# Kernel tuning notes

Measured on AMD Instinct MI355X. Metric: run time of the kernel, lower is better.

## Reference

```python
import jax, jax.numpy as jnp
import numpy as np

LN_EPS = 1e-5  # torch.nn.LayerNorm default


def setup_inputs() -> dict:
    key = jax.random.key(0)
    k1, k2 = jax.random.split(key)
    N, D_IN, D_OUT, G = 4096, 512, 512, 32
    x = jax.random.normal(k1, (N, D_IN), dtype=jnp.float32)
    ln_w = jnp.ones((D_IN,), dtype=jnp.float32)
    ln_b = jnp.zeros((D_IN,), dtype=jnp.float32)
    scale = 1.0 / (np.sqrt(D_IN) * np.sqrt(G))
    fouriercoeffs = jax.random.normal(k2, (2, D_OUT, D_IN, G), dtype=jnp.float32) * scale
    bias = jnp.zeros((1, D_OUT), dtype=jnp.float32)
    return {"x": x, "ln_w": ln_w, "ln_b": ln_b, "fouriercoeffs": fouriercoeffs, "bias": bias}


def reference(x, ln_w, ln_b, fouriercoeffs, bias):
    # LayerNorm over last dim
    mu = jnp.mean(x, axis=-1, keepdims=True)
    var = jnp.mean((x - mu) ** 2, axis=-1, keepdims=True)
    xn = (x - mu) * jax.lax.rsqrt(var + LN_EPS) * ln_w + ln_b
    G = fouriercoeffs.shape[-1]
    k = jnp.arange(1, G + 1, dtype=xn.dtype)           # [G]
    arg = xn[:, :, None] * k                            # [N, D_in, G]
    c = jnp.cos(arg)
    s = jnp.sin(arg)
    # contraction over (inputdim, gridsize) -> GEMM-shaped einsum
    y = jnp.einsum('big,oig->bo', c, fouriercoeffs[0])
    y = y + jnp.einsum('big,oig->bo', s, fouriercoeffs[1])
    y = y + bias
    return y
```

## Files before the change

### kernel.cpp

```cpp
#include <hip/hip_runtime.h>
#include <hip/hip_bf16.h>


#define N_ROWS 4096
#define D_IN   512
#define D_OUT  512
#define KT     16384
#define BM 128
#define BN 128
#define SPLITK 4

typedef short short8 __attribute__((ext_vector_type(8)));
typedef float float4v __attribute__((ext_vector_type(4)));

__device__ inline unsigned int pack2bf(float a, float b) {
    __hip_bfloat162 h = __float22bfloat162_rn(make_float2(a, b));
    union { __hip_bfloat162 h; unsigned int u; } cv;
    cv.h = h;
    return cv.u;
}

__device__ inline unsigned short bf16_1(float a) {
    union { float f; unsigned int u; } cv;
    cv.f = a;
    unsigned int r = (cv.u + 0x7fff + ((cv.u >> 16) & 1)) >> 16;
    return (unsigned short)r;
}

__global__ __launch_bounds__(256) void ln_stats(const float* __restrict__ x,
        float2* __restrict__ mu_rs) {
    const int t = threadIdx.x;
    const int row = blockIdx.x * 4 + (t >> 6);
    const int lane = t & 63;
    const float4* xr = (const float4*)(x + (size_t)row * D_IN);
    float4 a = xr[lane];
    float4 c = xr[lane + 64];
    float s = a.x + a.y + a.z + a.w + c.x + c.y + c.z + c.w;
    float q = a.x * a.x + a.y * a.y + a.z * a.z + a.w * a.w
            + c.x * c.x + c.y * c.y + c.z * c.z + c.w * c.w;
    #pragma unroll
    for (int off = 32; off > 0; off >>= 1) {
        s += __shfl_down(s, off, 64);
        q += __shfl_down(q, off, 64);
    }
    if (lane == 0) {
        float mu = s * (1.f / D_IN);
        float var = q * (1.f / D_IN) - mu * mu;
        mu_rs[row] = make_float2(mu, rsqrtf(var + 1e-5f));
    }
}

__global__ __launch_bounds__(256) void feat_seed(const float* __restrict__ x,
        const float* __restrict__ w, const float* __restrict__ b,
        const float2* __restrict__ mu_rs, float2* __restrict__ csT) {
    __shared__ float2 tile[64][65];
    const int t = threadIdx.x;
    const int r0 = blockIdx.x * 64, i0 = blockIdx.y * 64;
    const int rr = t >> 6;
    const int cc = t & 63;
    const float wv = w[i0 + cc], bv = b[i0 + cc];
    #pragma unroll
    for (int p = 0; p < 16; ++p) {
        const int row = r0 + p * 4 + rr;
        float v = x[(size_t)row * D_IN + i0 + cc];
        float2 mr = mu_rs[row];
        float xn = (v - mr.x) * mr.y * wv + bv;
        float sn, cn;
        __sincosf(xn, &sn, &cn);
        tile[p * 4 + rr][cc] = make_float2(cn, sn);
    }
    __syncthreads();
    #pragma unroll
    for (int p = 0; p < 16; ++p) {
        const int dim = p * 4 + rr;
        csT[(size_t)(i0 + dim) * N_ROWS + r0 + cc] = tile[cc][dim];
    }
}

__global__ __launch_bounds__(256) void cvt_kernel(const float* __restrict__ fc,
        unsigned short* __restrict__ Wb) {
    size_t e = ((size_t)blockIdx.x * 256 + threadIdx.x) * 8;
    const float4* in = (const float4*)(fc + e);
    float4 a = in[0];
    float4 c = in[1];
    uint4 o;
    o.x = pack2bf(a.x, a.y);
    o.y = pack2bf(a.z, a.w);
    o.z = pack2bf(c.x, c.y);
    o.w = pack2bf(c.z, c.w);
    *(uint4*)(Wb + e) = o;
}

__device__ inline void stage_feats(unsigned short* Abuf, float2 cs, int ttype,
                                   int frow, int ihalf) {
    const float c1 = cs.x, s1 = cs.y;
    const float c2 = c1 + c1;
    float prev = ttype ? 0.f : 1.f;
    float cur  = ttype ? s1 : c1;
    const int rbase = frow * 64;
    const int sw = frow & 7;
    unsigned int us[4];
    #pragma unroll
    for (int d = 0; d < 16; ++d) {
        float f0 = cur;
        float f1 = __builtin_fmaf(c2, cur, -prev);
        float f2 = __builtin_fmaf(c2, f1, -cur);
        prev = f1;
        cur = f2;
        us[d & 3] = pack2bf(f0, f1);
        if ((d & 3) == 3) {
            const int kc = ihalf * 4 + (d >> 2);
            *(uint4*)&Abuf[rbase + ((kc ^ sw) << 3)] =
                make_uint4(us[0], us[1], us[2], us[3]);
        }
    }
}

__device__ inline void gl_lds16(const unsigned short* gsrc, unsigned short* ldst) {
    __builtin_amdgcn_global_load_lds(
        (const __attribute__((address_space(1))) unsigned int*)gsrc,
        (__attribute__((address_space(3))) unsigned int*)ldst, 16, 0, 0);
}

__device__ inline void read_af(const unsigned short* As, short8 (&af)[2][4],
                               int wm, int lm, int lq, int swA) {
    #pragma unroll
    for (int h = 0; h < 2; ++h)
        #pragma unroll
        for (int tm = 0; tm < 4; ++tm)
            af[h][tm] = *(const short8*)
                &As[(wm + tm * 16 + lm) * 64 + (((h * 4 + lq) ^ swA) << 3)];
}

__device__ inline void read_bf(const unsigned short* Bp, short8 (&bf)[2][4],
                               int bBase) {
    #pragma unroll
    for (int h = 0; h < 2; ++h)
        #pragma unroll
        for (int tn = 0; tn < 4; ++tn)
            bf[h][tn] = *(const short8*)&Bp[bBase + tn * 1024 + h * 256];
}

__device__ inline void mfma_block(short8 (&af)[2][4], short8 (&bf)[2][4],
                                  float4v (&acc)[4][4]) {
    __builtin_amdgcn_s_setprio(1);
    #pragma unroll
    for (int h = 0; h < 2; ++h)
        #pragma unroll
        for (int tm = 0; tm < 4; ++tm)
            #pragma unroll
            for (int tn = 0; tn < 4; ++tn)
                acc[tm][tn] = __builtin_amdgcn_mfma_f32_16x16x32_bf16(
                    af[h][tm], bf[h][tn], acc[tm][tn], 0, 0, 0);
    __builtin_amdgcn_s_setprio(0);
}

__global__ __launch_bounds__(256, 2) void fkan_gemm(const float2* __restrict__ csT,
        const unsigned short* __restrict__ Wb, unsigned short* __restrict__ pb) {
    __shared__ unsigned short As[BM * 64];
    __shared__ unsigned short Bs[3][BN * 64];
    const int t = threadIdx.x;
    const int row0 = blockIdx.x * BM;
    const int col0 = blockIdx.y * BN;
    const int kz = blockIdx.z;
    const int k0 = kz * 4096;
    const int i0 = kz * 128;
    const int frow = t & 127;
    const int ihalf = t >> 7;
    const int l = t & 63, wv = t >> 6;
    const int wm = (wv & 1) * 64, wn = (wv >> 1) * 64;
    const int lm = l & 15, lq = l >> 4;
    const int c8 = l & 7, s8 = l >> 3;
    const unsigned short* Bg0 = Wb + (size_t)(col0 + wv * 32 + c8) * KT + k0 + s8 * 8;
    const int swA = lm & 7;
    const int bBase = ((wn >> 3) + (lm >> 3)) * 512 + lq * 64 + (lm & 7) * 8;

    const float2* csBase = csT + (size_t)(i0 + ihalf) * N_ROWS + row0 + frow;

    float4v acc[4][4];
    #pragma unroll
    for (int i = 0; i < 4; ++i)
        #pragma unroll
        for (int j = 0; j < 4; ++j)
            acc[i][j] = (float4v){0.f, 0.f, 0.f, 0.f};

    #pragma unroll
    for (int j = 0; j < 4; ++j)
        gl_lds16(Bg0 + (size_t)(j * 8) * KT, &Bs[0][(wv * 4 + j) * 512]);
    #pragma unroll
    for (int j = 0; j < 4; ++j)
        gl_lds16(Bg0 + 64 + (size_t)(j * 8) * KT, &Bs[1][(wv * 4 + j) * 512]);
    {
        float2 c0 = csBase[0];
        float2 tmp = csBase[2 * N_ROWS];
        stage_feats(As, c0, 0, frow, ihalf);
        asm volatile("s_waitcnt vmcnt(4) lgkmcnt(0)" ::: "memory");
        __builtin_amdgcn_s_barrier();
        float2 csA = tmp;
        int rd = 0, wr = 2;
        for (int it = 0; it < 126; ++it) {
            const unsigned short* Bp = &Bs[rd][0];
            short8 af[2][4];
            read_af(As, af, wm, lm, lq, swA);
            {
                const int in = it + 2;
                const unsigned short* gb =
                    Bg0 + (size_t)(in >> 6) * D_OUT * KT + (in & 63) * 64;
                #pragma unroll
                for (int j = 0; j < 4; ++j)
                    gl_lds16(gb + (size_t)(j * 8) * KT, &Bs[wr][(wv * 4 + j) * 512]);
            }
            asm volatile("s_waitcnt lgkmcnt(0)" ::: "memory");
            __builtin_amdgcn_s_barrier();
            float2 csN = csBase[(size_t)(((it + 2) & 63) * 2) * N_ROWS];
            stage_feats(As, csA, (it + 1) >> 6, frow, ihalf);
            csA = csN;
            short8 bf[2][4];
            read_bf(Bp, bf, bBase);
            mfma_block(af, bf, acc);
            asm volatile("s_waitcnt vmcnt(5) lgkmcnt(0)" ::: "memory");
            __builtin_amdgcn_s_barrier();
            rd = (rd == 2) ? 0 : rd + 1;
            wr = (wr == 2) ? 0 : wr + 1;
        }
        {
            const unsigned short* Bp = &Bs[0][0];
            short8 af[2][4];
            read_af(As, af, wm, lm, lq, swA);
            asm volatile("s_waitcnt lgkmcnt(0)" ::: "memory");
            __builtin_amdgcn_s_barrier();
            stage_feats(As, csA, 1, frow, ihalf);
            short8 bf[2][4];
            read_bf(Bp, bf, bBase);
            mfma_block(af, bf, acc);
            asm volatile("s_waitcnt vmcnt(0) lgkmcnt(0)" ::: "memory");
            __builtin_amdgcn_s_barrier();
        }
        {
            const unsigned short* Bp = &Bs[1][0];
            short8 af[2][4];
            read_af(As, af, wm, lm, lq, swA);
            short8 bf[2][4];
            read_bf(Bp, bf, bBase);
            mfma_block(af, bf, acc);
        }
    }
    unsigned short* pc = pb + (size_t)kz * N_ROWS * D_OUT;
    #pragma unroll
    for (int tm = 0; tm < 4; ++tm)
        #pragma unroll
        for (int tn = 0; tn < 4; ++tn)
            #pragma unroll
            for (int r = 0; r < 4; ++r) {
                const int row = row0 + wm + tm * 16 + lq * 4 + r;
                const int col = col0 + wn + tn * 16 + lm;
                pc[(size_t)row * D_OUT + col] = bf16_1(acc[tm][tn][r]);
            }
}

__global__ __launch_bounds__(256) void reduce_kernel(const unsigned short* __restrict__ pb,
        const float* __restrict__ bias, float* __restrict__ out) {
    const size_t e = ((size_t)blockIdx.x * 256 + threadIdx.x) * 4;
    const int col = (int)(e & (D_OUT - 1));
    float4 s = *(const float4*)(bias + col);
    #pragma unroll
    for (int c = 0; c < SPLITK; ++c) {
        ushort4 u = *(const ushort4*)(pb + (size_t)c * N_ROWS * D_OUT + e);
        union { unsigned int u; float f; } f0, f1, f2, f3;
        f0.u = (unsigned int)u.x << 16;
        f1.u = (unsigned int)u.y << 16;
        f2.u = (unsigned int)u.z << 16;
        f3.u = (unsigned int)u.w << 16;
        s.x += f0.f; s.y += f1.f; s.z += f2.f; s.w += f3.f;
    }
    *(float4*)(out + e) = s;
}

extern "C" void kernel_launch(void* const* d_in, const int* in_sizes, int n_in,
                              void* d_out, int out_size, void* d_ws, size_t ws_size,
                              hipStream_t stream) {
    const float* x    = (const float*)d_in[0];
    const float* ln_w = (const float*)d_in[1];
    const float* ln_b = (const float*)d_in[2];
    const float* fc   = (const float*)d_in[3];
    const float* bias = (const float*)d_in[4];
    float* out = (float*)d_out;

    float2* csT = (float2*)d_ws;
    float2* mu_rs = (float2*)((char*)d_ws + (16u << 20));
    unsigned short* Wb = (unsigned short*)((char*)d_ws + (17u << 20));
    unsigned short* pbp = (unsigned short*)((char*)d_ws + (51u << 20));

    ln_stats<<<N_ROWS / 4, 256, 0, stream>>>(x, mu_rs);
    feat_seed<<<dim3(N_ROWS / 64, D_IN / 64), 256, 0, stream>>>(x, ln_w, ln_b, mu_rs, csT);
    cvt_kernel<<<8192, 256, 0, stream>>>(fc, Wb);
    fkan_gemm<<<dim3(N_ROWS / BM, D_OUT / BN, SPLITK), 256, 0, stream>>>(csT, Wb, pbp);
    reduce_kernel<<<2048, 256, 0, stream>>>(pbp, bias, out);
}
```

Baseline: 288.7 us.

## Fuse preprocessing kernels, raise split-K to 8, double-buffer B with 3 blocks/CU

Merges LayerNorm stats, sin/cos seeding and the weight bf16 conversion into one pre_kernel, which removes two launches and the mu/rstd round trip. The GEMM moves from split-K 4 to 8 and from a triple-buffered B pipeline to a double-buffered one, with launch bounds allowing 3 blocks per CU. This shrinks LDS per block and doubles the grid to improve occupancy and latency hiding. In exchange, the reduce kernel reads twice as many bf16 partials, B prefetch depth drops to one stage, and the fused pre-kernel uses only 256 blocks.

```diff
diff --git a/kernel.cpp b/kernel.cpp
--- a/kernel.cpp
+++ b/kernel.cpp
@@ -8,7 +8,8 @@
 #define KT     16384
 #define BM 128
 #define BN 128
-#define SPLITK 4
+#define SPLITK 8
+#define NT 64
 
 typedef short short8 __attribute__((ext_vector_type(8)));
 typedef float float4v __attribute__((ext_vector_type(4)));
@@ -27,68 +28,63 @@
     return (unsigned short)r;
 }
 
-__global__ __launch_bounds__(256) void ln_stats(const float* __restrict__ x,
-        float2* __restrict__ mu_rs) {
+__global__ __launch_bounds__(256) void pre_kernel(const float* __restrict__ x,
+        const float* __restrict__ lnw, const float* __restrict__ lnb,
+        const float* __restrict__ fc, float2* __restrict__ csT,
+        unsigned short* __restrict__ Wb) {
+    __shared__ __align__(16) float xs[16 * 516];
+    __shared__ float2 murs[16];
     const int t = threadIdx.x;
-    const int row = blockIdx.x * 4 + (t >> 6);
-    const int lane = t & 63;
-    const float4* xr = (const float4*)(x + (size_t)row * D_IN);
-    float4 a = xr[lane];
-    float4 c = xr[lane + 64];
-    float s = a.x + a.y + a.z + a.w + c.x + c.y + c.z + c.w;
-    float q = a.x * a.x + a.y * a.y + a.z * a.z + a.w * a.w
-            + c.x * c.x + c.y * c.y + c.z * c.z + c.w * c.w;
-    #pragma unroll
-    for (int off = 32; off > 0; off >>= 1) {
-        s += __shfl_down(s, off, 64);
-        q += __shfl_down(q, off, 64);
-    }
-    if (lane == 0) {
-        float mu = s * (1.f / D_IN);
-        float var = q * (1.f / D_IN) - mu * mu;
-        mu_rs[row] = make_float2(mu, rsqrtf(var + 1e-5f));
-    }
-}
-
-__global__ __launch_bounds__(256) void feat_seed(const float* __restrict__ x,
-        const float* __restrict__ w, const float* __restrict__ b,
-        const float2* __restrict__ mu_rs, float2* __restrict__ csT) {
-    __shared__ float2 tile[64][65];
-    const int t = threadIdx.x;
-    const int r0 = blockIdx.x * 64, i0 = blockIdx.y * 64;
-    const int rr = t >> 6;
-    const int cc = t & 63;
-    const float wv = w[i0 + cc], bv = b[i0 + cc];
-    #pragma unroll
-    for (int p = 0; p < 16; ++p) {
-        const int row = r0 + p * 4 + rr;
-        float v = x[(size_t)row * D_IN + i0 + cc];
-        float2 mr = mu_rs[row];
-        float xn = (v - mr.x) * mr.y * wv + bv;
-        float sn, cn;
-        __sincosf(xn, &sn, &cn);
-        tile[p * 4 + rr][cc] = make_float2(cn, sn);
+    const int r0 = blockIdx.x * 16;
+    {
+        const int row = t >> 4, tq = t & 15;
+        const float* xr = x + (size_t)(r0 + row) * D_IN;
+        float s = 0.f, q = 0.f;
+        #pragma unroll
+        for (int k = 0; k < 8; ++k) {
+            float4 v = *(const float4*)(xr + tq * 4 + k * 64);
+            *(float4*)&xs[row * 516 + tq * 4 + k * 64] = v;
+            s += v.x + v.y + v.z + v.w;
+            q += v.x * v.x + v.y * v.y + v.z * v.z + v.w * v.w;
+        }
+        #pragma unroll
+        for (int off = 8; off > 0; off >>= 1) {
+            s += __shfl_xor(s, off, 16);
+            q += __shfl_xor(q, off, 16);
+        }
+        if (tq == 0) {
+            float mu = s * (1.f / D_IN);
+            float var = q * (1.f / D_IN) - mu * mu;
+            murs[row] = make_float2(mu, rsqrtf(var + 1e-5f));
+        }
     }
     __syncthreads();
-    #pragma unroll
-    for (int p = 0; p < 16; ++p) {
-        const int dim = p * 4 + rr;
-        csT[(size_t)(i0 + dim) * N_ROWS + r0 + cc] = tile[cc][dim];
-    }
-}
-
-__global__ __launch_bounds__(256) void cvt_kernel(const float* __restrict__ fc,
-        unsigned short* __restrict__ Wb) {
-    size_t e = ((size_t)blockIdx.x * 256 + threadIdx.x) * 8;
-    const float4* in = (const float4*)(fc + e);
-    float4 a = in[0];
-    float4 c = in[1];
-    uint4 o;
-    o.x = pack2bf(a.x, a.y);
-    o.y = pack2bf(a.z, a.w);
-    o.z = pack2bf(c.x, c.y);
-    o.w = pack2bf(c.z, c.w);
-    *(uint4*)(Wb + e) = o;
+    {
+        const int brow = t & 15, dimg = t >> 4;
+        const float2 mr = murs[brow];
+        #pragma unroll 4
+        for (int j = 0; j < 32; ++j) {
+            const int dim = j * 16 + dimg;
+            float xv = xs[brow * 516 + dim];
+            float xn = (xv - mr.x) * mr.y * lnw[dim] + lnb[dim];
+            float s1, c1;
+            __sincosf(xn, &s1, &c1);
+            csT[(size_t)dim * N_ROWS + r0 + brow] = make_float2(c1, s1);
+        }
+    }
+    {
+        size_t e = ((size_t)blockIdx.x * 256 + t) * 8;
+        for (int it2 = 0; it2 < 32; ++it2, e += (size_t)256 * 256 * 8) {
+            const float4* in = (const float4*)(fc + e);
+            float4 a = in[0], c = in[1];
+            uint4 o;
+            o.x = pack2bf(a.x, a.y);
+            o.y = pack2bf(a.z, a.w);
+            o.z = pack2bf(c.x, c.y);
+            o.w = pack2bf(c.z, c.w);
+            *(uint4*)(Wb + e) = o;
+        }
+    }
 }
 
 __device__ inline void stage_feats(unsigned short* Abuf, float2 cs, int ttype,
@@ -155,16 +151,16 @@
     __builtin_amdgcn_s_setprio(0);
 }
 
-__global__ __launch_bounds__(256, 2) void fkan_gemm(const float2* __restrict__ csT,
+__global__ __launch_bounds__(256, 3) void fkan_gemm(const float2* __restrict__ csT,
         const unsigned short* __restrict__ Wb, unsigned short* __restrict__ pb) {
     __shared__ unsigned short As[BM * 64];
-    __shared__ unsigned short Bs[3][BN * 64];
+    __shared__ unsigned short Bs[2][BN * 64];
     const int t = threadIdx.x;
     const int row0 = blockIdx.x * BM;
     const int col0 = blockIdx.y * BN;
     const int kz = blockIdx.z;
-    const int k0 = kz * 4096;
-    const int i0 = kz * 128;
+    const int k0 = kz * 2048;
+    const int i0 = kz * 64;
     const int frow = t & 127;
     const int ihalf = t >> 7;
     const int l = t & 63, wv = t >> 6;
@@ -184,66 +180,48 @@
         for (int j = 0; j < 4; ++j)
             acc[i][j] = (float4v){0.f, 0.f, 0.f, 0.f};
 
+    float2 cs0 = csBase[0];
     #pragma unroll
     for (int j = 0; j < 4; ++j)
         gl_lds16(Bg0 + (size_t)(j * 8) * KT, &Bs[0][(wv * 4 + j) * 512]);
-    #pragma unroll
-    for (int j = 0; j < 4; ++j)
-        gl_lds16(Bg0 + 64 + (size_t)(j * 8) * KT, &Bs[1][(wv * 4 + j) * 512]);
-    {
-        float2 c0 = csBase[0];
-        float2 tmp = csBase[2 * N_ROWS];
-        stage_feats(As, c0, 0, frow, ihalf);
-        asm volatile("s_waitcnt vmcnt(4) lgkmcnt(0)" ::: "memory");
+    __builtin_amdgcn_sched_barrier(0);
+    float2 csA = csBase[2 * N_ROWS];
+    stage_feats(As, cs0, 0, frow, ihalf);
+    asm volatile("s_waitcnt vmcnt(1) lgkmcnt(0)" ::: "memory");
+    __builtin_amdgcn_s_barrier();
+
+    #pragma unroll 1
+    for (int it = 0; it < NT - 1; ++it) {
+        const int p = it & 1;
+        short8 af[2][4];
+        read_af(As, af, wm, lm, lq, swA);
+        {
+            const int n = it + 1;
+            const unsigned short* gb =
+                Bg0 + (size_t)(n >> 5) * D_OUT * KT + (n & 31) * 64;
+            unsigned short* ldst = &Bs[p ^ 1][(wv * 4) * 512];
+            #pragma unroll
+            for (int j = 0; j < 4; ++j)
+                gl_lds16(gb + (size_t)(j * 8) * KT, ldst + j * 512);
+        }
+        __builtin_amdgcn_sched_barrier(0);
+        float2 csN = csBase[(size_t)(((it + 2) & 31) * 2) * N_ROWS];
+        asm volatile("s_waitcnt lgkmcnt(0)" ::: "memory");
         __builtin_amdgcn_s_barrier();
-        float2 csA = tmp;
-        int rd = 0, wr = 2;
-        for (int it = 0; it < 126; ++it) {
-            const unsigned short* Bp = &Bs[rd][0];
-            short8 af[2][4];
-            read_af(As, af, wm, lm, lq, swA);
-            {
-                const int in = it + 2;
-                const unsigned short* gb =
-                    Bg0 + (size_t)(in >> 6) * D_OUT * KT + (in & 63) * 64;
-                #pragma unroll
-                for (int j = 0; j < 4; ++j)
-                    gl_lds16(gb + (size_t)(j * 8) * KT, &Bs[wr][(wv * 4 + j) * 512]);
-            }
-            asm volatile("s_waitcnt lgkmcnt(0)" ::: "memory");
-            __builtin_amdgcn_s_barrier();
-            float2 csN = csBase[(size_t)(((it + 2) & 63) * 2) * N_ROWS];
-            stage_feats(As, csA, (it + 1) >> 6, frow, ihalf);
-            csA = csN;
-            short8 bf[2][4];
-            read_bf(Bp, bf, bBase);
-            mfma_block(af, bf, acc);
-            asm volatile("s_waitcnt vmcnt(5) lgkmcnt(0)" ::: "memory");
-            __builtin_amdgcn_s_barrier();
-            rd = (rd == 2) ? 0 : rd + 1;
-            wr = (wr == 2) ? 0 : wr + 1;
-        }
-        {
-            const unsigned short* Bp = &Bs[0][0];
-            short8 af[2][4];
-            read_af(As, af, wm, lm, lq, swA);
-            asm volatile("s_waitcnt lgkmcnt(0)" ::: "memory");
-            __builtin_amdgcn_s_barrier();
-            stage_feats(As, csA, 1, frow, ihalf);
-            short8 bf[2][4];
-            read_bf(Bp, bf, bBase);
-            mfma_block(af, bf, acc);
-            asm volatile("s_waitcnt vmcnt(0) lgkmcnt(0)" ::: "memory");
-            __builtin_amdgcn_s_barrier();
-        }
-        {
-            const unsigned short* Bp = &Bs[1][0];
-            short8 af[2][4];
-            read_af(As, af, wm, lm, lq, swA);
-            short8 bf[2][4];
-            read_bf(Bp, bf, bBase);
-            mfma_block(af, bf, acc);
-        }
+        stage_feats(As, csA, (it + 1) >> 5, frow, ihalf);
+        csA = csN;
+        short8 bf[2][4];
+        read_bf(&Bs[p][0], bf, bBase);
+        mfma_block(af, bf, acc);
+        asm volatile("s_waitcnt vmcnt(1) lgkmcnt(0)" ::: "memory");
+        __builtin_amdgcn_s_barrier();
+    }
+    {
+        short8 af[2][4];
+        read_af(As, af, wm, lm, lq, swA);
+        short8 bf[2][4];
+        read_bf(&Bs[1][0], bf, bBase);
+        mfma_block(af, bf, acc);
     }
     unsigned short* pc = pb + (size_t)kz * N_ROWS * D_OUT;
     #pragma unroll
@@ -287,13 +265,10 @@
     float* out = (float*)d_out;
 
     float2* csT = (float2*)d_ws;
-    float2* mu_rs = (float2*)((char*)d_ws + (16u << 20));
-    unsigned short* Wb = (unsigned short*)((char*)d_ws + (17u << 20));
-    unsigned short* pbp = (unsigned short*)((char*)d_ws + (51u << 20));
-
-    ln_stats<<<N_ROWS / 4, 256, 0, stream>>>(x, mu_rs);
-    feat_seed<<<dim3(N_ROWS / 64, D_IN / 64), 256, 0, stream>>>(x, ln_w, ln_b, mu_rs, csT);
-    cvt_kernel<<<8192, 256, 0, stream>>>(fc, Wb);
+    unsigned short* Wb = (unsigned short*)((char*)d_ws + (16u << 20));
+    unsigned short* pbp = (unsigned short*)((char*)d_ws + (48u << 20));
+
+    pre_kernel<<<256, 256, 0, stream>>>(x, ln_w, ln_b, fc, csT, Wb);
     fkan_gemm<<<dim3(N_ROWS / BM, D_OUT / BN, SPLITK), 256, 0, stream>>>(csT, Wb, pbp);
     reduce_kernel<<<2048, 256, 0, stream>>>(pbp, bias, out);
 }
```

Measured after the change: 295.4 us. 1.02x slower.
